# Kernel tuning notes

Hardware: AMD Instinct MI355X
Metric: run time of the kernel (lower is better)

The kernel has to match this reference:

```python
import jax, jax.numpy as jnp
import numpy as np

LORA_ALPHA = 32.0
LORA_RANK = 16
SCALE = LORA_ALPHA / LORA_RANK


def setup_inputs() -> dict:
    key = jax.random.key(0)
    k1, k2, k3, k4, k5 = jax.random.split(key, 5)
    B, S, D_IN, D_OUT, R = 4, 2048, 4096, 4096, LORA_RANK
    x = jax.random.normal(k1, (B, S, D_IN), dtype=jnp.float32)
    weight = jax.random.normal(k2, (D_OUT, D_IN), dtype=jnp.float32) * (1.0 / np.sqrt(D_IN))
    bias = jax.random.normal(k3, (D_OUT,), dtype=jnp.float32)
    lora_A = jax.random.normal(k4, (B, D_IN, R), dtype=jnp.float32) * (1.0 / np.sqrt(D_IN))
    lora_B = jax.random.normal(k5, (B, R, D_OUT), dtype=jnp.float32) * 0.01
    return {"x": x, "weight": weight, "bias": bias, "lora_A": lora_A, "lora_B": lora_B}


def reference(x, weight, bias, lora_A, lora_B):
    # base: F.linear(x, weight, bias) -> x @ W^T + b
    base = jnp.einsum('bsi,oi->bso', x, weight) + bias
    # per-sample low-rank correction (the expand+bmm path, without materializing
    # the expanded [B*S, d, r] tensors):
    low = jnp.einsum('bsi,bir->bsr', x, lora_A)        # [B, S, r]
    lora_out = jnp.einsum('bsr,bro->bso', low, lora_B)  # [B, S, d_out]
    return base + lora_out * SCALE
```

## Files before the change

kernel.cpp:

```cpp
#include <hip/hip_runtime.h>
#include <hip/hip_bf16.h>
#include <stdint.h>

typedef __bf16 bf16_t;
typedef __bf16 bf16x8 __attribute__((ext_vector_type(8)));
typedef float f32x4 __attribute__((ext_vector_type(4)));

#define M_ROWS 8192
#define N_COLS 4096
#define K_DIM  4096
#define KEXT   64
#define BM 256
#define BN 256
#define BK 64
#define NT 65

#define XBF_BYTES (67108864ull)
#define WBF_BYTES (33554432ull)
#define LOW_BYTES (1048576ull)
#define LBT_BYTES (2097152ull)

__device__ __forceinline__ void gload16(const void* g, void* l) {
    __builtin_amdgcn_global_load_lds(
        (const __attribute__((address_space(1))) unsigned int*)g,
        (__attribute__((address_space(3))) unsigned int*)l, 16, 0, 0);
}

__global__ __launch_bounds__(256) void prep_kernel(
    const float* __restrict__ x, const float* __restrict__ lA,
    const float* __restrict__ lB, const float* __restrict__ weight,
    bf16_t* __restrict__ Xbf, bf16_t* __restrict__ Wbf,
    bf16_t* __restrict__ lowbf, bf16_t* __restrict__ lBt)
{
    const int blk = blockIdx.x;
    const int tid = threadIdx.x;

    if (blk < 512) {
        const int m0   = blk * 16;
        const int batch = m0 >> 11;
        const int rg   = tid >> 6;
        const int lane = tid & 63;
        const float* lAb = lA + (size_t)batch * (K_DIM * 16);

        f32x4 acc4[4][4];
        #pragma unroll
        for (int i = 0; i < 4; ++i)
            #pragma unroll
            for (int j = 0; j < 4; ++j)
                acc4[i][j] = (f32x4)0.0f;

        #pragma unroll 1
        for (int kc = 0; kc < 8; ++kc) {
            const int k0 = kc * 512 + lane * 8;
            float xs[4][8];
            #pragma unroll
            for (int rr = 0; rr < 4; ++rr) {
                const int m = m0 + rg * 4 + rr;
                const float* xp = x + (size_t)m * K_DIM + k0;
                const f32x4 a = *(const f32x4*)xp;
                const f32x4 b = *(const f32x4*)(xp + 4);
                bf16x8 v;
                v[0]=(bf16_t)a[0]; v[1]=(bf16_t)a[1]; v[2]=(bf16_t)a[2]; v[3]=(bf16_t)a[3];
                v[4]=(bf16_t)b[0]; v[5]=(bf16_t)b[1]; v[6]=(bf16_t)b[2]; v[7]=(bf16_t)b[3];
                *(bf16x8*)(Xbf + (size_t)m * K_DIM + k0) = v;
                xs[rr][0]=a[0]; xs[rr][1]=a[1]; xs[rr][2]=a[2]; xs[rr][3]=a[3];
                xs[rr][4]=b[0]; xs[rr][5]=b[1]; xs[rr][6]=b[2]; xs[rr][7]=b[3];
            }
            #pragma unroll
            for (int j = 0; j < 8; ++j) {
                const f32x4* lr = (const f32x4*)(lAb + (size_t)(k0 + j) * 16);
                const f32x4 l0 = lr[0], l1 = lr[1], l2 = lr[2], l3 = lr[3];
                #pragma unroll
                for (int rr = 0; rr < 4; ++rr) {
                    const float xv = xs[rr][j];
                    acc4[rr][0] += xv * l0;
                    acc4[rr][1] += xv * l1;
                    acc4[rr][2] += xv * l2;
                    acc4[rr][3] += xv * l3;
                }
            }
        }

        #pragma unroll
        for (int off = 32; off >= 1; off >>= 1) {
            #pragma unroll
            for (int rr = 0; rr < 4; ++rr)
                #pragma unroll
                for (int g = 0; g < 4; ++g)
                    #pragma unroll
                    for (int q = 0; q < 4; ++q)
                        acc4[rr][g][q] += __shfl_xor(acc4[rr][g][q], off, 64);
        }

        const int rr_w = lane >> 4, rw = lane & 15;
        float outv = 0.0f;
        #pragma unroll
        for (int rr = 0; rr < 4; ++rr)
            #pragma unroll
            for (int g = 0; g < 4; ++g)
                #pragma unroll
                for (int q = 0; q < 4; ++q)
                    if (rr == rr_w && (g * 4 + q) == rw) outv = acc4[rr][g][q];
        lowbf[(size_t)(m0 + rg * 4 + rr_w) * KEXT + rw] = (bf16_t)outv;

        if (tid < 96) {
            bf16x8 z;
            #pragma unroll
            for (int i = 0; i < 8; ++i) z[i] = (bf16_t)0.0f;
            const int row = m0 + tid / 6;
            const int c0  = 16 + (tid % 6) * 8;
            *(bf16x8*)(lowbf + (size_t)row * KEXT + c0) = z;
        }
    } else if (blk < 1536) {
        const long long i0 = (long long)(blk - 512) * 256 + tid;
        #pragma unroll 1
        for (int it = 0; it < 8; ++it) {
            const long long i = i0 + (long long)it * 262144;
            const f32x4* s = (const f32x4*)(weight + i * 8);
            const f32x4 a = s[0], b = s[1];
            bf16x8 v;
            v[0]=(bf16_t)a[0]; v[1]=(bf16_t)a[1]; v[2]=(bf16_t)a[2]; v[3]=(bf16_t)a[3];
            v[4]=(bf16_t)b[0]; v[5]=(bf16_t)b[1]; v[6]=(bf16_t)b[2]; v[7]=(bf16_t)b[3];
            *(bf16x8*)(Wbf + i * 8) = v;
        }
    } else {
        const int idx = (blk - 1536) * 256 + tid;
        const int b = idx >> 12, n = idx & 4095;
        const float* src = lB + (size_t)b * (16 * N_COLS) + n;
        bf16_t* dst = lBt + ((size_t)b * N_COLS + n) * KEXT;
        bf16x8 v0, v1, z;
        #pragma unroll
        for (int r = 0; r < 8; ++r) {
            v0[r] = (bf16_t)(2.0f * src[(size_t)r * N_COLS]);
            v1[r] = (bf16_t)(2.0f * src[(size_t)(8 + r) * N_COLS]);
            z[r]  = (bf16_t)0.0f;
        }
        *(bf16x8*)(dst)      = v0;
        *(bf16x8*)(dst + 8)  = v1;
        #pragma unroll
        for (int c = 16; c < 64; c += 8)
            *(bf16x8*)(dst + c) = z;
    }
}

__device__ __forceinline__ void read_a(bf16x8 (&d)[2][4], const char* base,
                                       int rowB, const int (&swz)[2]) {
    #pragma unroll
    for (int kk = 0; kk < 2; ++kk)
        #pragma unroll
        for (int mi = 0; mi < 4; ++mi)
            d[kk][mi] = *(const bf16x8*)(base + rowB + mi * 2048 + swz[kk]);
}
__device__ __forceinline__ void read_b(bf16x8 (&d)[2][2], const char* base,
                                       int rowB, const int (&swz)[2]) {
    #pragma unroll
    for (int kk = 0; kk < 2; ++kk)
        #pragma unroll
        for (int ni = 0; ni < 2; ++ni)
            d[kk][ni] = *(const bf16x8*)(base + rowB + ni * 2048 + swz[kk]);
}
template<int R0, int C0>
__device__ __forceinline__ void mfma_q(f32x4 (&acc)[8][4],
                                       const bf16x8 (&af)[2][4],
                                       const bf16x8 (&bf)[2][2]) {
    #pragma unroll
    for (int kk = 0; kk < 2; ++kk)
        #pragma unroll
        for (int mi = 0; mi < 4; ++mi)
            #pragma unroll
            for (int ni = 0; ni < 2; ++ni)
                acc[R0 + mi][C0 + ni] = __builtin_amdgcn_mfma_f32_16x16x32_bf16(
                    af[kk][mi], bf[kk][ni], acc[R0 + mi][C0 + ni], 0, 0, 0);
}

__global__ __launch_bounds__(512, 1) void gemm_lora_kernel(
    const bf16_t* __restrict__ Xbf, const bf16_t* __restrict__ Wbf,
    const bf16_t* __restrict__ lowbf, const bf16_t* __restrict__ lBt,
    const float* __restrict__ bias, float* __restrict__ out)
{
    __shared__ __align__(16) char lds[131072];

    int wg = blockIdx.x;
    const int cpx = gridDim.x >> 3;
    wg = (wg & 7) * cpx + (wg >> 3);

    const int nbn  = N_COLS / BN;
    const int brow = (wg / nbn) * BM;
    const int bcol = (wg % nbn) * BN;
    const int batch = brow >> 11;

    const int tid  = threadIdx.x;
    const int lane = tid & 63;
    const int w    = tid >> 6;
    const int wr   = w >> 2;
    const int wc   = w & 3;

    const int srow   = tid >> 3;
    const int bphys  = (tid & 7) * 16;
    const int colOff = (bphys ^ ((srow & 7) << 4)) >> 1;

    const bf16_t* aSrc = Xbf + (size_t)(brow + srow) * K_DIM + colOff;
    const bf16_t* bSrc = Wbf + (size_t)(bcol + srow) * K_DIM + colOff;
    const bf16_t* aExt = lowbf + (size_t)(brow + srow) * KEXT + colOff;
    const bf16_t* bExt = lBt + ((size_t)batch * N_COLS + bcol + srow) * KEXT + colOff;

    auto stageAu = [&](int tau, int u) {
        char* dst = lds + (tau & 1) * 65536 + u * 8192 + tid * 16;
        if (tau < NT - 1) gload16(aSrc + (size_t)(u * 64) * K_DIM + tau * BK, dst);
        else              gload16(aExt + (size_t)(u * 64) * KEXT, dst);
    };
    auto stageBh = [&](int tau, int h) {
        char* dst = lds + (tau & 1) * 65536 + 32768 + h * 16384 + tid * 16;
        if (tau < NT - 1) {
            const bf16_t* s = bSrc + (size_t)(h * 128) * K_DIM + tau * BK;
            gload16(s, dst);
            gload16(s + (size_t)64 * K_DIM, dst + 8192);
        } else {
            const bf16_t* s = bExt + (size_t)(h * 128) * KEXT;
            gload16(s, dst);
            gload16(s + 64 * KEXT, dst + 8192);
        }
    };

    const int aRowB = (wr * 128 + (lane & 15)) * 128;
    const int bRowB = (wc * 64 + (lane & 15)) * 128;
    const int swz[2] = { (((lane >> 4) * 16) ^ ((lane & 7) << 4)),
                         ((64 + (lane >> 4) * 16) ^ ((lane & 7) << 4)) };

    f32x4 acc[8][4];
    #pragma unroll
    for (int i = 0; i < 8; ++i)
        #pragma unroll
        for (int j = 0; j < 4; ++j)
            acc[i][j] = (f32x4)0.0f;

    bf16x8 a0F[2][4], a1F[2][4], b1F[2][2], b0Fa[2][2], b0Fb[2][2];

    stageAu(0, 0); stageAu(0, 1); stageAu(0, 2); stageAu(0, 3);
    stageBh(0, 0); stageBh(0, 1);
    stageAu(1, 0); stageAu(1, 2); stageBh(1, 0); stageAu(1, 1); stageAu(1, 3);
    asm volatile("s_waitcnt vmcnt(6)" ::: "memory");
    __builtin_amdgcn_s_barrier();
    read_a(a0F, lds, aRowB, swz);
    read_b(b0Fa, lds + 32768, bRowB, swz);

#define ITER(T, CUR, NXT, B0C, B0N) do {                                      \
    const char* AbC = lds + (CUR) * 65536;                                    \
    const char* BbC = AbC + 32768;                                            \
    const char* AbN = lds + (NXT) * 65536;                                    \
    const char* BbN = AbN + 32768;                                            \
                                             \
    if ((T) + 1 <= 64) stageBh((T) + 1, 1);                                   \
    __builtin_amdgcn_s_barrier();                                             \
    asm volatile("s_waitcnt lgkmcnt(0)" ::: "memory");                        \
    __builtin_amdgcn_s_setprio(1);                                            \
    read_b(b1F, BbC + 4096, bRowB, swz);                                      \
    mfma_q<0, 0>(acc, a0F, B0C);                                              \
    __builtin_amdgcn_s_setprio(0);                                            \
    __builtin_amdgcn_s_barrier();                                             \
                                             \
    if ((T) + 2 <= 64) { stageAu((T) + 2, 0); stageAu((T) + 2, 2); }          \
    __builtin_amdgcn_s_barrier();                                             \
    asm volatile("s_waitcnt lgkmcnt(0)" ::: "memory");                        \
    __builtin_amdgcn_s_setprio(1);                                            \
    read_a(a1F, AbC + 8192, aRowB, swz);                                      \
    mfma_q<0, 2>(acc, a0F, b1F);                                              \
    __builtin_amdgcn_s_setprio(0);                                            \
    __builtin_amdgcn_s_barrier();                                             \
                       \
    if ((T) + 2 <= 64) stageBh((T) + 2, 0);                                   \
    __builtin_amdgcn_s_barrier();                                             \
    asm volatile("s_waitcnt lgkmcnt(0)" ::: "memory");                        \
    __builtin_amdgcn_s_setprio(1);                                            \
    mfma_q<4, 2>(acc, a1F, b1F);                                              \
    __builtin_amdgcn_s_setprio(0);                                            \
    __builtin_amdgcn_s_barrier();                                             \
     \
    if ((T) + 2 <= 64) { stageAu((T) + 2, 1); stageAu((T) + 2, 3); }          \
    if ((T) < 63) { asm volatile("s_waitcnt vmcnt(6)" ::: "memory"); }        \
    else          { asm volatile("s_waitcnt vmcnt(0)" ::: "memory"); }        \
    __builtin_amdgcn_s_barrier();                                             \
    __builtin_amdgcn_s_setprio(1);                                            \
    if ((T) < 64) { read_a(a0F, AbN, aRowB, swz);                             \
                    read_b(B0N, BbN, bRowB, swz); }                           \
    mfma_q<4, 0>(acc, a1F, B0C);                                              \
    __builtin_amdgcn_s_setprio(0);                                            \
    __builtin_amdgcn_s_barrier();                                             \
} while (0)

    #pragma unroll 1
    for (int t = 0; t < 64; t += 2) {
        ITER(t,     0, 1, b0Fa, b0Fb);
        ITER(t + 1, 1, 0, b0Fb, b0Fa);
    }
    ITER(64, 0, 1, b0Fa, b0Fb);
#undef ITER

    const int cl = lane & 15;
    const int r0 = (lane >> 4) * 4;
    float bv[4];
    #pragma unroll
    for (int nh = 0; nh < 2; ++nh)
        #pragma unroll
        for (int ni = 0; ni < 2; ++ni)
            bv[nh * 2 + ni] = bias[bcol + wc * 64 + nh * 32 + ni * 16 + cl];
    #pragma unroll
    for (int mh = 0; mh < 2; ++mh)
        #pragma unroll
        for (int mi = 0; mi < 4; ++mi) {
            const int row = brow + wr * 128 + mh * 64 + mi * 16 + r0;
            #pragma unroll
            for (int nh = 0; nh < 2; ++nh)
                #pragma unroll
                for (int ni = 0; ni < 2; ++ni) {
                    const int col = bcol + wc * 64 + nh * 32 + ni * 16 + cl;
                    float* op = out + (size_t)row * N_COLS + col;
                    const f32x4 v = acc[mh * 4 + mi][nh * 2 + ni];
                    const float bb = bv[nh * 2 + ni];
                    #pragma unroll
                    for (int r = 0; r < 4; ++r)
                        op[(size_t)r * N_COLS] = v[r] + bb;
                }
        }
}

extern "C" void kernel_launch(void* const* d_in, const int* in_sizes, int n_in,
                              void* d_out, int out_size, void* d_ws, size_t ws_size,
                              hipStream_t stream) {
    const float* x      = (const float*)d_in[0];
    const float* weight = (const float*)d_in[1];
    const float* bias   = (const float*)d_in[2];
    const float* lora_A = (const float*)d_in[3];
    const float* lora_B = (const float*)d_in[4];
    float* out = (float*)d_out;

    if (ws_size < XBF_BYTES + WBF_BYTES + LOW_BYTES + LBT_BYTES) return;

    char* ws = (char*)d_ws;
    bf16_t* Xbf  = (bf16_t*)ws;
    bf16_t* Wbf  = (bf16_t*)(ws + XBF_BYTES);
    bf16_t* lowb = (bf16_t*)(ws + XBF_BYTES + WBF_BYTES);
    bf16_t* lBt  = (bf16_t*)(ws + XBF_BYTES + WBF_BYTES + LOW_BYTES);

    prep_kernel<<<1600, 256, 0, stream>>>(x, lora_A, lora_B, weight,
                                          Xbf, Wbf, lowb, lBt);
    gemm_lora_kernel<<<512, 512, 0, stream>>>(Xbf, Wbf, lowb, lBt, bias, out);
}
```

Baseline: 346.8 us.

## Compute LoRA low-rank projection with bf16 MFMA in separate kernel

Removes the fp32 scalar x·A reduction with its shuffle tree from the prep kernel, which now just converts x to bf16 and transposes lora_A to bf16. A new small kernel computes x·A from the bf16 copy of x using MFMA instructions, split over K halves and combined through LDS. This adds a third launch and re-reads Xbf, and it lowers the precision of the low-rank projection to bf16 inputs. The GEMM loop also moves its LDS fragment reads ahead of the s_setprio raise.

```diff
diff --git a/kernel.cpp b/kernel.cpp
--- a/kernel.cpp
+++ b/kernel.cpp
@@ -19,6 +19,7 @@
 #define WBF_BYTES (33554432ull)
 #define LOW_BYTES (1048576ull)
 #define LBT_BYTES (2097152ull)
+#define LAT_BYTES (524288ull)
 
 __device__ __forceinline__ void gload16(const void* g, void* l) {
     __builtin_amdgcn_global_load_lds(
@@ -30,86 +31,22 @@
     const float* __restrict__ x, const float* __restrict__ lA,
     const float* __restrict__ lB, const float* __restrict__ weight,
     bf16_t* __restrict__ Xbf, bf16_t* __restrict__ Wbf,
-    bf16_t* __restrict__ lowbf, bf16_t* __restrict__ lBt)
+    bf16_t* __restrict__ lBt, bf16_t* __restrict__ lAT)
 {
     const int blk = blockIdx.x;
     const int tid = threadIdx.x;
 
     if (blk < 512) {
-        const int m0   = blk * 16;
-        const int batch = m0 >> 11;
-        const int rg   = tid >> 6;
-        const int lane = tid & 63;
-        const float* lAb = lA + (size_t)batch * (K_DIM * 16);
-
-        f32x4 acc4[4][4];
-        #pragma unroll
-        for (int i = 0; i < 4; ++i)
-            #pragma unroll
-            for (int j = 0; j < 4; ++j)
-                acc4[i][j] = (f32x4)0.0f;
-
+        const long long i0 = (long long)blk * 256 + tid;
         #pragma unroll 1
-        for (int kc = 0; kc < 8; ++kc) {
-            const int k0 = kc * 512 + lane * 8;
-            float xs[4][8];
-            #pragma unroll
-            for (int rr = 0; rr < 4; ++rr) {
-                const int m = m0 + rg * 4 + rr;
-                const float* xp = x + (size_t)m * K_DIM + k0;
-                const f32x4 a = *(const f32x4*)xp;
-                const f32x4 b = *(const f32x4*)(xp + 4);
-                bf16x8 v;
-                v[0]=(bf16_t)a[0]; v[1]=(bf16_t)a[1]; v[2]=(bf16_t)a[2]; v[3]=(bf16_t)a[3];
-                v[4]=(bf16_t)b[0]; v[5]=(bf16_t)b[1]; v[6]=(bf16_t)b[2]; v[7]=(bf16_t)b[3];
-                *(bf16x8*)(Xbf + (size_t)m * K_DIM + k0) = v;
-                xs[rr][0]=a[0]; xs[rr][1]=a[1]; xs[rr][2]=a[2]; xs[rr][3]=a[3];
-                xs[rr][4]=b[0]; xs[rr][5]=b[1]; xs[rr][6]=b[2]; xs[rr][7]=b[3];
-            }
-            #pragma unroll
-            for (int j = 0; j < 8; ++j) {
-                const f32x4* lr = (const f32x4*)(lAb + (size_t)(k0 + j) * 16);
-                const f32x4 l0 = lr[0], l1 = lr[1], l2 = lr[2], l3 = lr[3];
-                #pragma unroll
-                for (int rr = 0; rr < 4; ++rr) {
-                    const float xv = xs[rr][j];
-                    acc4[rr][0] += xv * l0;
-                    acc4[rr][1] += xv * l1;
-                    acc4[rr][2] += xv * l2;
-                    acc4[rr][3] += xv * l3;
-                }
-            }
-        }
-
-        #pragma unroll
-        for (int off = 32; off >= 1; off >>= 1) {
-            #pragma unroll
-            for (int rr = 0; rr < 4; ++rr)
-                #pragma unroll
-                for (int g = 0; g < 4; ++g)
-                    #pragma unroll
-                    for (int q = 0; q < 4; ++q)
-                        acc4[rr][g][q] += __shfl_xor(acc4[rr][g][q], off, 64);
-        }
-
-        const int rr_w = lane >> 4, rw = lane & 15;
-        float outv = 0.0f;
-        #pragma unroll
-        for (int rr = 0; rr < 4; ++rr)
-            #pragma unroll
-            for (int g = 0; g < 4; ++g)
-                #pragma unroll
-                for (int q = 0; q < 4; ++q)
-                    if (rr == rr_w && (g * 4 + q) == rw) outv = acc4[rr][g][q];
-        lowbf[(size_t)(m0 + rg * 4 + rr_w) * KEXT + rw] = (bf16_t)outv;
-
-        if (tid < 96) {
-            bf16x8 z;
-            #pragma unroll
-            for (int i = 0; i < 8; ++i) z[i] = (bf16_t)0.0f;
-            const int row = m0 + tid / 6;
-            const int c0  = 16 + (tid % 6) * 8;
-            *(bf16x8*)(lowbf + (size_t)row * KEXT + c0) = z;
+        for (int it = 0; it < 32; ++it) {
+            const long long i = i0 + (long long)it * 131072;
+            const f32x4* s = (const f32x4*)(x + i * 8);
+            const f32x4 a = s[0], b = s[1];
+            bf16x8 v;
+            v[0]=(bf16_t)a[0]; v[1]=(bf16_t)a[1]; v[2]=(bf16_t)a[2]; v[3]=(bf16_t)a[3];
+            v[4]=(bf16_t)b[0]; v[5]=(bf16_t)b[1]; v[6]=(bf16_t)b[2]; v[7]=(bf16_t)b[3];
+            *(bf16x8*)(Xbf + i * 8) = v;
         }
     } else if (blk < 1536) {
         const long long i0 = (long long)(blk - 512) * 256 + tid;
@@ -123,7 +60,7 @@
             v[4]=(bf16_t)b[0]; v[5]=(bf16_t)b[1]; v[6]=(bf16_t)b[2]; v[7]=(bf16_t)b[3];
             *(bf16x8*)(Wbf + i * 8) = v;
         }
-    } else {
+    } else if (blk < 1600) {
         const int idx = (blk - 1536) * 256 + tid;
         const int b = idx >> 12, n = idx & 4095;
         const float* src = lB + (size_t)b * (16 * N_COLS) + n;
@@ -135,11 +72,69 @@
             v1[r] = (bf16_t)(2.0f * src[(size_t)(8 + r) * N_COLS]);
             z[r]  = (bf16_t)0.0f;
         }
-        *(bf16x8*)(dst)      = v0;
-        *(bf16x8*)(dst + 8)  = v1;
+        *(bf16x8*)(dst)     = v0;
+        *(bf16x8*)(dst + 8) = v1;
         #pragma unroll
         for (int c = 16; c < 64; c += 8)
             *(bf16x8*)(dst + c) = z;
+    } else {
+        const int q = blk - 1600;
+        const int b = q >> 4, c = q & 15;
+        const float* src = lA + (size_t)b * (K_DIM * 16) + c;
+        bf16_t* dst = lAT + ((size_t)b * 16 + c) * K_DIM + tid * 16;
+        bf16x8 v0, v1;
+        #pragma unroll
+        for (int j = 0; j < 8; ++j) {
+            v0[j] = (bf16_t)src[(size_t)(tid * 16 + j) * 16];
+            v1[j] = (bf16_t)src[(size_t)(tid * 16 + 8 + j) * 16];
+        }
+        *(bf16x8*)(dst)     = v0;
+        *(bf16x8*)(dst + 8) = v1;
+    }
+}
+
+__global__ __launch_bounds__(256) void lowg_kernel(
+    const bf16_t* __restrict__ Xbf, const bf16_t* __restrict__ lAT,
+    bf16_t* __restrict__ lowbf)
+{
+    __shared__ f32x4 lsum[128];
+    const int tid  = threadIdx.x;
+    const int w    = tid >> 6;
+    const int lane = tid & 63;
+    const int rowg = w >> 1, khalf = w & 1;
+    const int m0   = blockIdx.x * 32;
+    const int batch = m0 >> 11;
+    const int r16  = lane & 15;
+    const int kg   = lane >> 4;
+
+    const bf16_t* aB = Xbf + (size_t)(m0 + rowg * 16 + r16) * K_DIM + khalf * 2048 + kg * 8;
+    const bf16_t* bB = lAT + ((size_t)batch * 16 + r16) * K_DIM + khalf * 2048 + kg * 8;
+
+    f32x4 acc0 = (f32x4)0.0f, acc1 = (f32x4)0.0f;
+    #pragma unroll 4
+    for (int ks = 0; ks < 32; ++ks) {
+        acc0 = __builtin_amdgcn_mfma_f32_16x16x32_bf16(
+            *(const bf16x8*)(aB + ks * 64), *(const bf16x8*)(bB + ks * 64), acc0, 0, 0, 0);
+        acc1 = __builtin_amdgcn_mfma_f32_16x16x32_bf16(
+            *(const bf16x8*)(aB + ks * 64 + 32), *(const bf16x8*)(bB + ks * 64 + 32), acc1, 0, 0, 0);
+    }
+    f32x4 s = acc0 + acc1;
+    if (khalf == 1) lsum[rowg * 64 + lane] = s;
+    __syncthreads();
+    if (khalf == 0) {
+        s += lsum[rowg * 64 + lane];
+        const int m = m0 + rowg * 16 + kg * 4;
+        #pragma unroll
+        for (int ri = 0; ri < 4; ++ri)
+            lowbf[(size_t)(m + ri) * KEXT + r16] = (bf16_t)s[ri];
+    }
+    if (tid < 192) {
+        bf16x8 z;
+        #pragma unroll
+        for (int i = 0; i < 8; ++i) z[i] = (bf16_t)0.0f;
+        const int row = m0 + tid / 6;
+        const int c0  = 16 + (tid % 6) * 8;
+        *(bf16x8*)(lowbf + (size_t)row * KEXT + c0) = z;
     }
 }
 
@@ -253,8 +248,8 @@
     if ((T) + 1 <= 64) stageBh((T) + 1, 1);                                   \
     __builtin_amdgcn_s_barrier();                                             \
     asm volatile("s_waitcnt lgkmcnt(0)" ::: "memory");                        \
+    read_b(b1F, BbC + 4096, bRowB, swz);                                      \
     __builtin_amdgcn_s_setprio(1);                                            \
-    read_b(b1F, BbC + 4096, bRowB, swz);                                      \
     mfma_q<0, 0>(acc, a0F, B0C);                                              \
     __builtin_amdgcn_s_setprio(0);                                            \
     __builtin_amdgcn_s_barrier();                                             \
@@ -262,12 +257,12 @@
     if ((T) + 2 <= 64) { stageAu((T) + 2, 0); stageAu((T) + 2, 2); }          \
     __builtin_amdgcn_s_barrier();                                             \
     asm volatile("s_waitcnt lgkmcnt(0)" ::: "memory");                        \
+    read_a(a1F, AbC + 8192, aRowB, swz);                                      \
     __builtin_amdgcn_s_setprio(1);                                            \
-    read_a(a1F, AbC + 8192, aRowB, swz);                                      \
     mfma_q<0, 2>(acc, a0F, b1F);                                              \
     __builtin_amdgcn_s_setprio(0);                                            \
     __builtin_amdgcn_s_barrier();                                             \
-                       \
+                                                        \
     if ((T) + 2 <= 64) stageBh((T) + 2, 0);                                   \
     __builtin_amdgcn_s_barrier();                                             \
     asm volatile("s_waitcnt lgkmcnt(0)" ::: "memory");                        \
@@ -275,14 +270,14 @@
     mfma_q<4, 2>(acc, a1F, b1F);                                              \
     __builtin_amdgcn_s_setprio(0);                                            \
     __builtin_amdgcn_s_barrier();                                             \
-     \
+               \
     if ((T) + 2 <= 64) { stageAu((T) + 2, 1); stageAu((T) + 2, 3); }          \
     if ((T) < 63) { asm volatile("s_waitcnt vmcnt(6)" ::: "memory"); }        \
     else          { asm volatile("s_waitcnt vmcnt(0)" ::: "memory"); }        \
     __builtin_amdgcn_s_barrier();                                             \
-    __builtin_amdgcn_s_setprio(1);                                            \
     if ((T) < 64) { read_a(a0F, AbN, aRowB, swz);                             \
                     read_b(B0N, BbN, bRowB, swz); }                           \
+    __builtin_amdgcn_s_setprio(1);                                            \
     mfma_q<4, 0>(acc, a1F, B0C);                                              \
     __builtin_amdgcn_s_setprio(0);                                            \
     __builtin_amdgcn_s_barrier();                                             \
@@ -334,15 +329,17 @@
     const float* lora_B = (const float*)d_in[4];
     float* out = (float*)d_out;
 
-    if (ws_size < XBF_BYTES + WBF_BYTES + LOW_BYTES + LBT_BYTES) return;
+    if (ws_size < XBF_BYTES + WBF_BYTES + LOW_BYTES + LBT_BYTES + LAT_BYTES) return;
 
     char* ws = (char*)d_ws;
     bf16_t* Xbf  = (bf16_t*)ws;
     bf16_t* Wbf  = (bf16_t*)(ws + XBF_BYTES);
     bf16_t* lowb = (bf16_t*)(ws + XBF_BYTES + WBF_BYTES);
     bf16_t* lBt  = (bf16_t*)(ws + XBF_BYTES + WBF_BYTES + LOW_BYTES);
-
-    prep_kernel<<<1600, 256, 0, stream>>>(x, lora_A, lora_B, weight,
-                                          Xbf, Wbf, lowb, lBt);
+    bf16_t* lAT  = (bf16_t*)(ws + XBF_BYTES + WBF_BYTES + LOW_BYTES + LBT_BYTES);
+
+    prep_kernel<<<1664, 256, 0, stream>>>(x, lora_A, lora_B, weight,
+                                          Xbf, Wbf, lBt, lAT);
+    lowg_kernel<<<256, 256, 0, stream>>>(Xbf, lAT, lowb);
     gemm_lora_kernel<<<512, 512, 0, stream>>>(Xbf, Wbf, lowb, lBt, bias, out);
 }
```

Result: faster. 322.5 us (-7.0%).
